# Performance work log

Hardware: AMD Instinct MI355X
Metric: run time of the kernel (lower is better)

## Reference

```python
import jax, jax.numpy as jnp
import numpy as np

NEG = -1e30  # stand-in for -inf; rows always have >=1 valid entry


def setup_inputs() -> dict:
    key = jax.random.key(0)
    ks = jax.random.split(key, 7)
    C, E, O = 256, 256, 256
    x = jax.random.normal(ks[0], (4, C, 64, 64), dtype=jnp.float32)
    # 1x1 conv weights stored as (out, in) matrices
    Wq = jax.random.normal(ks[1], (E, C), dtype=jnp.float32) * (1.0 / np.sqrt(C))
    bq = jax.random.normal(ks[2], (E,), dtype=jnp.float32) * 0.01
    Wkv = jax.random.normal(ks[3], (E + O, C), dtype=jnp.float32) * (1.0 / np.sqrt(C))
    bkv = jax.random.normal(ks[4], (E + O,), dtype=jnp.float32) * 0.01
    Wp = jax.random.normal(ks[5], (O, O), dtype=jnp.float32) * (1.0 / np.sqrt(O))
    bp = jax.random.normal(ks[6], (O,), dtype=jnp.float32) * 0.01
    return {"x": x, "Wq": Wq, "bq": bq, "Wkv": Wkv, "bkv": bkv, "Wp": Wp, "bp": bp, "n_heads": 8}


def _heads(t, n_heads):
    # (N, C, S) -> (N, n_heads, S, C//n_heads)
    n, c, s = t.shape
    return t.reshape(n, n_heads, c // n_heads, s).transpose(0, 1, 3, 2)


def reference(x, Wq, bq, Wkv, bkv, Wp, bp, n_heads):
    n, c, h, w = x.shape
    S = h * w
    E = Wq.shape[0]
    O = Wkv.shape[0] - E
    xf = x.reshape(n, c, S)  # (N, C, S)

    q = jnp.einsum('oc,ncs->nos', Wq, xf) + bq[:, None]
    kv = jnp.einsum('oc,ncs->nos', Wkv, xf) + bkv[:, None]
    k, v = kv[:, :E], kv[:, E:]

    q = _heads(q, n_heads)  # (N, H, S, dq)
    k = _heads(k, n_heads)
    v = _heads(v, n_heads)  # (N, H, S, dv)

    head_dim = E // n_heads
    # causal mask: tril with diagonal=0 (mask_center=False -> pixel attends to itself)
    mask = jnp.tril(jnp.ones((S, S), dtype=bool), k=0)

    attn = jnp.einsum('nhqd,nhkd->nhqk', q, k) / np.sqrt(head_dim)
    attn = jnp.where(mask, attn, NEG)
    attn = jax.nn.softmax(attn, axis=-1)
    attn = jnp.where(mask, attn, 0.0)

    out = jnp.einsum('nhqk,nhkd->nhqd', attn, v)  # (N, H, S, dv)
    out = out.transpose(0, 1, 3, 2).reshape(n, O, S)  # (N, O, S)
    out = jnp.einsum('oc,ncs->nos', Wp, out) + bp[:, None]
    return out.reshape(n, O, h, w)
```

## Files before the change

kernel.cpp:

```cpp
#include <hip/hip_runtime.h>

typedef __bf16 bf16x8 __attribute__((ext_vector_type(8)));
typedef float f32x4 __attribute__((ext_vector_type(4)));
typedef float f32x16 __attribute__((ext_vector_type(16)));

#define S_LEN 4096

__device__ __forceinline__ unsigned short f2bf(float f) {
    unsigned int u = __float_as_uint(f);
    u += 0x7fffu + ((u >> 16) & 1u);
    return (unsigned short)(u >> 16);
}

__device__ __forceinline__ unsigned int pk_bf16(float lo, float hi) {
    unsigned int r;
    asm("v_cvt_pk_bf16_f32 %0, %1, %2" : "=v"(r) : "v"(lo), "v"(hi));
    return r;
}

__global__ __launch_bounds__(256) void k_xt(const float* __restrict__ x, unsigned short* __restrict__ xT,
                                            const float* __restrict__ Wq, const float* __restrict__ Wkv,
                                            const float* __restrict__ Wp, unsigned short* __restrict__ wb,
                                            unsigned short* __restrict__ wpb) {
    __shared__ unsigned short tile[64 * 80];
    const int tid = threadIdx.x;
    if (blockIdx.z == 4) {
        const int bi = blockIdx.x + 64 * blockIdx.y;
        for (int i = bi * 256 + tid; i < 262144; i += 65536) {
            if (i < 65536)       wb[i]           = f2bf(Wq[i]);
            else if (i < 196608) wb[i]           = f2bf(Wkv[i - 65536]);
            else                 wpb[i - 196608] = f2bf(Wp[i - 196608]);
        }
        return;
    }
    const int b = blockIdx.z, c0 = blockIdx.y * 64, s0 = blockIdx.x * 64;
#pragma unroll
    for (int ii = 0; ii < 4; ++ii) {
        int flat = ii * 256 + tid;
        int cr = flat >> 4, s4 = flat & 15;
        const float4 v = *(const float4*)(x + ((size_t)(b * 256 + c0 + cr)) * S_LEN + s0 + s4 * 4);
        tile[(s4 * 4 + 0) * 80 + cr] = f2bf(v.x);
        tile[(s4 * 4 + 1) * 80 + cr] = f2bf(v.y);
        tile[(s4 * 4 + 2) * 80 + cr] = f2bf(v.z);
        tile[(s4 * 4 + 3) * 80 + cr] = f2bf(v.w);
    }
    __syncthreads();
#pragma unroll
    for (int ii = 0; ii < 2; ++ii) {
        int flat = ii * 256 + tid;
        int sr = flat >> 3, ch = flat & 7;
        uint4 u = *(const uint4*)&tile[sr * 80 + ch * 8];
        *(uint4*)(xT + ((size_t)(b * 4096 + s0 + sr)) * 256 + c0 + ch * 8) = u;
    }
}

__global__ __launch_bounds__(256) void k_qkv(const unsigned short* __restrict__ wb,
                                             const unsigned short* __restrict__ xT,
                                             const float* __restrict__ bq,
                                             const float* __restrict__ bkv,
                                             unsigned short* __restrict__ qws,
                                             unsigned short* __restrict__ kws,
                                             unsigned short* __restrict__ vws) {
    __shared__ unsigned short As[128 * 32];
    __shared__ unsigned short Bs[128 * 32];
    const int b = blockIdx.z;
    const int o0 = blockIdx.y * 128, s0 = blockIdx.x * 128;
    const int tid = threadIdx.x;
    const int w = tid >> 6, l = tid & 63, g = l >> 4, lc = l & 15;
    const int wr = w >> 1, wc = w & 1;
    const unsigned short* xb = xT + (size_t)b * 4096 * 256;
    const float SM_C = 0.25505654458f;

    f32x4 acc[4][4];
#pragma unroll
    for (int m = 0; m < 4; ++m)
#pragma unroll
        for (int nf = 0; nf < 4; ++nf) acc[m][nf] = (f32x4)(0.f);

    const int lrow = tid >> 1, lhalf = tid & 1;
    const int lsw0 = (lrow * 64 + lhalf * 32) ^ ((lrow & 7) << 4);
    const int lsw1 = (lrow * 64 + lhalf * 32 + 16) ^ ((lrow & 7) << 4);

    for (int kk = 0; kk < 8; ++kk) {
        const int c0 = kk * 32;
        __syncthreads();
        {
            const uint4* srcA = (const uint4*)(wb + (size_t)(o0 + lrow) * 256 + c0 + lhalf * 16);
            uint4 a0 = srcA[0], a1 = srcA[1];
            const uint4* srcB = (const uint4*)(xb + (size_t)(s0 + lrow) * 256 + c0 + lhalf * 16);
            uint4 b0 = srcB[0], b1 = srcB[1];
            *(uint4*)((char*)As + lsw0) = a0;
            *(uint4*)((char*)As + lsw1) = a1;
            *(uint4*)((char*)Bs + lsw0) = b0;
            *(uint4*)((char*)Bs + lsw1) = b1;
        }
        __syncthreads();
        bf16x8 af[4], bfv[4];
#pragma unroll
        for (int m = 0; m < 4; ++m) {
            int row = wr * 64 + m * 16 + lc;
            af[m] = *(const bf16x8*)((char*)As + ((row * 64 + g * 16) ^ ((row & 7) << 4)));
        }
#pragma unroll
        for (int nf = 0; nf < 4; ++nf) {
            int row = wc * 64 + nf * 16 + lc;
            bfv[nf] = *(const bf16x8*)((char*)Bs + ((row * 64 + g * 16) ^ ((row & 7) << 4)));
        }
#pragma unroll
        for (int m = 0; m < 4; ++m)
#pragma unroll
            for (int nf = 0; nf < 4; ++nf)
                acc[m][nf] = __builtin_amdgcn_mfma_f32_16x16x32_bf16(af[m], bfv[nf], acc[m][nf], 0, 0, 0);
    }

#pragma unroll
    for (int m = 0; m < 4; ++m)
#pragma unroll
        for (int nf = 0; nf < 4; ++nf)
#pragma unroll
            for (int i = 0; i < 4; ++i) {
                int o = o0 + wr * 64 + m * 16 + g * 4 + i;
                int s = s0 + wc * 64 + nf * 16 + lc;
                if (o < 256) {
                    int h = o >> 5, d = o & 31;
                    qws[(((size_t)(b * 8 + h)) * 4096 + s) * 32 + d] = f2bf((acc[m][nf][i] + bq[o]) * SM_C);
                } else if (o < 512) {
                    int oo = o - 256, h = oo >> 5, d = oo & 31;
                    kws[(((size_t)(b * 8 + h)) * 4096 + s) * 32 + d] = f2bf(acc[m][nf][i] + bkv[o - 256]);
                } else {
                    int oo = o - 512, h = oo >> 5, d = oo & 31;
                    vws[(size_t)(b * 8 + h) * 131072 + (((s >> 7) * 32 + d) << 7) + (s & 127)] =
                        f2bf(acc[m][nf][i] + bkv[o - 256]);
                }
            }
}

#define VC_STRIDE 544
#define BUF_STRIDE 8704

__device__ __forceinline__ void attn_sub(const unsigned short* __restrict__ kw_bh, int key0,
                                         const char* __restrict__ vbuf, int c,
                                         bf16x8 qf0, bf16x8 qf1, const f32x16& zf, bf16x8 ones,
                                         int lane31, int hh, bool domask,
                                         f32x16& o, f32x16& sums) {
    const unsigned short* kp = kw_bh + (size_t)(key0 + lane31) * 32 + hh * 8;
    bf16x8 kf0 = *(const bf16x8*)(kp);
    bf16x8 kf1 = *(const bf16x8*)(kp + 16);
    bf16x8 vf0 = *(const bf16x8*)(vbuf + (c * 4 + hh) * VC_STRIDE + lane31 * 16);
    bf16x8 vf1 = *(const bf16x8*)(vbuf + (c * 4 + 2 + hh) * VC_STRIDE + lane31 * 16);

    f32x16 s = __builtin_amdgcn_mfma_f32_32x32x16_bf16(kf0, qf0, zf, 0, 0, 0);
    s = __builtin_amdgcn_mfma_f32_32x32x16_bf16(kf1, qf1, s, 0, 0, 0);

    if (domask) {
#pragma unroll
        for (int r = 0; r < 16; ++r) {
            int krel = (r & 3) + 8 * (r >> 2) + 4 * hh;
            if (krel > lane31) s[r] = -1e30f;
        }
    }

    float p[16];
#pragma unroll
    for (int r = 0; r < 16; ++r) p[r] = __builtin_amdgcn_exp2f(s[r]);

    unsigned int c00 = pk_bf16(p[0], p[1]),   c01 = pk_bf16(p[2], p[3]);
    unsigned int c10 = pk_bf16(p[4], p[5]),   c11 = pk_bf16(p[6], p[7]);
    unsigned int c20 = pk_bf16(p[8], p[9]),   c21 = pk_bf16(p[10], p[11]);
    unsigned int c30 = pk_bf16(p[12], p[13]), c31 = pk_bf16(p[14], p[15]);
    asm("v_permlane32_swap_b32 %0, %1" : "+v"(c00), "+v"(c10));
    asm("v_permlane32_swap_b32 %0, %1" : "+v"(c01), "+v"(c11));
    asm("v_permlane32_swap_b32 %0, %1" : "+v"(c20), "+v"(c30));
    asm("v_permlane32_swap_b32 %0, %1" : "+v"(c21), "+v"(c31));
    union U { uint4 u; bf16x8 v; };
    U pa0, pa1;
    pa0.u = make_uint4(c00, c01, c10, c11);
    pa1.u = make_uint4(c20, c21, c30, c31);

    sums = __builtin_amdgcn_mfma_f32_32x32x16_bf16(ones, pa0.v, sums, 0, 0, 0);
    sums = __builtin_amdgcn_mfma_f32_32x32x16_bf16(ones, pa1.v, sums, 0, 0, 0);
    o = __builtin_amdgcn_mfma_f32_32x32x16_bf16(vf0, pa0.v, o, 0, 0, 0);
    o = __builtin_amdgcn_mfma_f32_32x32x16_bf16(vf1, pa1.v, o, 0, 0, 0);
}

__global__ __launch_bounds__(256, 4) void k_attn(const unsigned short* __restrict__ qw,
                                                 const unsigned short* __restrict__ kw,
                                                 const unsigned short* __restrict__ vw,
                                                 unsigned short* __restrict__ att) {
    __shared__ __align__(16) char smem[2 * BUF_STRIDE];

    const int tid = threadIdx.x;
    const int w = tid >> 6, l = tid & 63;
    const int lane31 = l & 31, hh = l >> 5;

    const int B = blockIdx.x;
    const int xcd = B & 7, idx = B >> 3;
    const int bh = xcd * 4 + (idx & 3);
    const int v4 = idx >> 2;
    const int j4 = v4 >> 3, d4 = v4 & 7;
    const int mt = (j4 & 1) ? (31 - 8 * (j4 >> 1) - d4) : (8 * (j4 >> 1) + d4);

    const int q = mt * 128 + w * 32 + lane31;

    const unsigned short* qw_bh = qw + (size_t)bh * 4096 * 32;
    const unsigned short* kw_bh = kw + (size_t)bh * 4096 * 32;
    const unsigned short* vw_bh = vw + (size_t)bh * 131072;

    const bf16x8 qf0 = *(const bf16x8*)(qw_bh + (size_t)q * 32 + hh * 8);
    const bf16x8 qf1 = *(const bf16x8*)(qw_bh + (size_t)q * 32 + hh * 8 + 16);

    const unsigned short* vsrc = vw_bh + tid * 16;
    const int vd0 = ((tid & 7) * 2) * VC_STRIDE + (tid >> 3) * 16;

    f32x16 o, sums, zf;
#pragma unroll
    for (int r = 0; r < 16; ++r) { o[r] = 0.f; sums[r] = 0.f; zf[r] = 0.f; }

    union OU { unsigned int u[4]; bf16x8 v; };
    OU onesU;
#pragma unroll
    for (int jj = 0; jj < 4; ++jj) onesU.u[jj] = 0x3F803F80u;
    const bf16x8 ones = onesU.v;

    {
        uint4 va = *(const uint4*)(vsrc);
        uint4 vbb = *(const uint4*)(vsrc + 8);
        *(uint4*)(smem + vd0)             = va;
        *(uint4*)(smem + vd0 + VC_STRIDE) = vbb;
    }

    int cur = 0;
    for (int r = 0; r < mt; ++r) {
        const unsigned short* vp = vsrc + (size_t)(r + 1) * 4096;
        uint4 va = *(const uint4*)(vp);
        uint4 vbb = *(const uint4*)(vp + 8);

        __syncthreads();
        const char* vbuf = smem + cur * BUF_STRIDE;
        const int k0 = r * 128;
        attn_sub(kw_bh, k0,      vbuf, 0, qf0, qf1, zf, ones, lane31, hh, false, o, sums);
        attn_sub(kw_bh, k0 + 32, vbuf, 1, qf0, qf1, zf, ones, lane31, hh, false, o, sums);
        attn_sub(kw_bh, k0 + 64, vbuf, 2, qf0, qf1, zf, ones, lane31, hh, false, o, sums);
        attn_sub(kw_bh, k0 + 96, vbuf, 3, qf0, qf1, zf, ones, lane31, hh, false, o, sums);

        char* nb = smem + (cur ^ 1) * BUF_STRIDE;
        *(uint4*)(nb + vd0)             = va;
        *(uint4*)(nb + vd0 + VC_STRIDE) = vbb;
        cur ^= 1;
    }

    __syncthreads();
    {
        const char* vbuf = smem + cur * BUF_STRIDE;
        const int k0 = mt * 128;
#pragma unroll
        for (int c = 0; c < 4; ++c)
            if (c <= w)
                attn_sub(kw_bh, k0 + 32 * c, vbuf, c, qf0, qf1, zf, ones, lane31, hh, c == w, o, sums);
    }

    const float inv = 1.0f / sums[0];
    unsigned int* dst = (unsigned int*)(att + (((size_t)(bh >> 3)) * 4096 + q) * 256 + (bh & 7) * 32);
#pragma unroll
    for (int jj = 0; jj < 8; ++jj) {
        unsigned int v = pk_bf16(o[2 * jj] * inv, o[2 * jj + 1] * inv);
        dst[(jj & 1) + 4 * (jj >> 1) + 2 * hh] = v;
    }
}

__global__ __launch_bounds__(256) void k_proj(const unsigned short* __restrict__ wpb,
                                              const unsigned short* __restrict__ att,
                                              const float* __restrict__ bp,
                                              float* __restrict__ out) {
    __shared__ unsigned short As[128 * 32];
    __shared__ unsigned short Bs[128 * 32];
    const int b = blockIdx.z;
    const int o0 = blockIdx.y * 128, s0 = blockIdx.x * 128;
    const int tid = threadIdx.x;
    const int w = tid >> 6, l = tid & 63, g = l >> 4, lc = l & 15;
    const int wr = w >> 1, wc = w & 1;
    const unsigned short* ab = att + (size_t)b * 4096 * 256;

    f32x4 acc[4][4];
#pragma unroll
    for (int m = 0; m < 4; ++m)
#pragma unroll
        for (int nf = 0; nf < 4; ++nf) acc[m][nf] = (f32x4)(0.f);

    const int lrow = tid >> 1, lhalf = tid & 1;
    const int lsw0 = (lrow * 64 + lhalf * 32) ^ ((lrow & 7) << 4);
    const int lsw1 = (lrow * 64 + lhalf * 32 + 16) ^ ((lrow & 7) << 4);

    for (int kk = 0; kk < 8; ++kk) {
        const int c0 = kk * 32;
        __syncthreads();
        {
            const uint4* srcA = (const uint4*)(wpb + (size_t)(o0 + lrow) * 256 + c0 + lhalf * 16);
            uint4 a0 = srcA[0], a1 = srcA[1];
            const uint4* srcB = (const uint4*)(ab + (size_t)(s0 + lrow) * 256 + c0 + lhalf * 16);
            uint4 b0 = srcB[0], b1 = srcB[1];
            *(uint4*)((char*)As + lsw0) = a0;
            *(uint4*)((char*)As + lsw1) = a1;
            *(uint4*)((char*)Bs + lsw0) = b0;
            *(uint4*)((char*)Bs + lsw1) = b1;
        }
        __syncthreads();
        bf16x8 af[4], bfv[4];
#pragma unroll
        for (int m = 0; m < 4; ++m) {
            int row = wr * 64 + m * 16 + lc;
            af[m] = *(const bf16x8*)((char*)As + ((row * 64 + g * 16) ^ ((row & 7) << 4)));
        }
#pragma unroll
        for (int nf = 0; nf < 4; ++nf) {
            int row = wc * 64 + nf * 16 + lc;
            bfv[nf] = *(const bf16x8*)((char*)Bs + ((row * 64 + g * 16) ^ ((row & 7) << 4)));
        }
#pragma unroll
        for (int m = 0; m < 4; ++m)
#pragma unroll
            for (int nf = 0; nf < 4; ++nf)
                acc[m][nf] = __builtin_amdgcn_mfma_f32_16x16x32_bf16(af[m], bfv[nf], acc[m][nf], 0, 0, 0);
    }

#pragma unroll
    for (int m = 0; m < 4; ++m)
#pragma unroll
        for (int nf = 0; nf < 4; ++nf)
#pragma unroll
            for (int i = 0; i < 4; ++i) {
                int o = o0 + wr * 64 + m * 16 + g * 4 + i;
                int s = s0 + wc * 64 + nf * 16 + lc;
                out[((size_t)(b * 256 + o)) * 4096 + s] = acc[m][nf][i] + bp[o];
            }
}

extern "C" void kernel_launch(void* const* d_in, const int* in_sizes, int n_in,
                              void* d_out, int out_size, void* d_ws, size_t ws_size,
                              hipStream_t stream) {
    const float* x   = (const float*)d_in[0];
    const float* Wq  = (const float*)d_in[1];
    const float* bq  = (const float*)d_in[2];
    const float* Wkv = (const float*)d_in[3];
    const float* bkv = (const float*)d_in[4];
    const float* Wp  = (const float*)d_in[5];
    const float* bp  = (const float*)d_in[6];
    float* out = (float*)d_out;
    char* ws = (char*)d_ws;

    unsigned short* wb  = (unsigned short*)(ws);
    unsigned short* wpb = (unsigned short*)(ws + 393216);
    unsigned short* xT  = (unsigned short*)(ws + 524288);
    unsigned short* qws = (unsigned short*)(ws + 8912896);
    unsigned short* kws = (unsigned short*)(ws + 17301504);
    unsigned short* vws = (unsigned short*)(ws + 25690112);
    unsigned short* att = (unsigned short*)(ws + 34078720);

    hipLaunchKernelGGL(k_xt, dim3(64, 4, 5), dim3(256), 0, stream, x, xT, Wq, Wkv, Wp, wb, wpb);
    hipLaunchKernelGGL(k_qkv, dim3(32, 6, 4), dim3(256), 0, stream, wb, xT, bq, bkv, qws, kws, vws);
    hipLaunchKernelGGL(k_attn, dim3(1024), dim3(256), 0, stream, qws, kws, vws, att);
    hipLaunchKernelGGL(k_proj, dim3(32, 2, 4), dim3(256), 0, stream, wpb, att, bp, out);
}
```

Measured before the change: 119.1 us.

## Process two V tiles per barrier and batch K fragment loads per round

The attention loop now stages two 128-key V tiles per shared-memory slot, halving the number of __syncthreads barriers per query tile, and handles an odd leftover tile in the tail. K fragments for a whole 128-key round are loaded up front into registers before the MFMA chain, so global-load latency overlaps more compute. LDS use doubles to about 34 KB per block and register pressure rises from the eight held K fragments, which may reduce occupancy under the 4-blocks-per-SM launch bound.

New measurement: 112.3 us, median of 2. -5.7%, faster.

```diff
diff --git a/kernel.cpp b/kernel.cpp
--- a/kernel.cpp
+++ b/kernel.cpp
@@ -136,16 +136,14 @@
 }
 
 #define VC_STRIDE 544
-#define BUF_STRIDE 8704
-
-__device__ __forceinline__ void attn_sub(const unsigned short* __restrict__ kw_bh, int key0,
+#define HALF_STRIDE 8704
+#define SLOT_STRIDE 17408
+
+__device__ __forceinline__ void attn_sub(bf16x8 kf0, bf16x8 kf1,
                                          const char* __restrict__ vbuf, int c,
                                          bf16x8 qf0, bf16x8 qf1, const f32x16& zf, bf16x8 ones,
                                          int lane31, int hh, bool domask,
                                          f32x16& o, f32x16& sums) {
-    const unsigned short* kp = kw_bh + (size_t)(key0 + lane31) * 32 + hh * 8;
-    bf16x8 kf0 = *(const bf16x8*)(kp);
-    bf16x8 kf1 = *(const bf16x8*)(kp + 16);
     bf16x8 vf0 = *(const bf16x8*)(vbuf + (c * 4 + hh) * VC_STRIDE + lane31 * 16);
     bf16x8 vf1 = *(const bf16x8*)(vbuf + (c * 4 + 2 + hh) * VC_STRIDE + lane31 * 16);
 
@@ -183,11 +181,28 @@
     o = __builtin_amdgcn_mfma_f32_32x32x16_bf16(vf1, pa1.v, o, 0, 0, 0);
 }
 
+__device__ __forceinline__ void attn_round_full(const unsigned short* __restrict__ kw_bh, int k0,
+                                                const char* __restrict__ vhalf,
+                                                bf16x8 qf0, bf16x8 qf1, const f32x16& zf, bf16x8 ones,
+                                                int lane31, int hh,
+                                                f32x16& o, f32x16& sums) {
+    const unsigned short* kp = kw_bh + (size_t)(k0 + lane31) * 32 + hh * 8;
+    bf16x8 kf[8];
+#pragma unroll
+    for (int c = 0; c < 4; ++c) {
+        kf[2 * c]     = *(const bf16x8*)(kp + c * 1024);
+        kf[2 * c + 1] = *(const bf16x8*)(kp + c * 1024 + 16);
+    }
+#pragma unroll
+    for (int c = 0; c < 4; ++c)
+        attn_sub(kf[2 * c], kf[2 * c + 1], vhalf, c, qf0, qf1, zf, ones, lane31, hh, false, o, sums);
+}
+
 __global__ __launch_bounds__(256, 4) void k_attn(const unsigned short* __restrict__ qw,
                                                  const unsigned short* __restrict__ kw,
                                                  const unsigned short* __restrict__ vw,
                                                  unsigned short* __restrict__ att) {
-    __shared__ __align__(16) char smem[2 * BUF_STRIDE];
+    __shared__ __align__(16) char smem[2 * SLOT_STRIDE];
 
     const int tid = threadIdx.x;
     const int w = tid >> 6, l = tid & 63;
@@ -201,6 +216,7 @@
     const int mt = (j4 & 1) ? (31 - 8 * (j4 >> 1) - d4) : (8 * (j4 >> 1) + d4);
 
     const int q = mt * 128 + w * 32 + lane31;
+    const int D = (mt + 2) >> 1;
 
     const unsigned short* qw_bh = qw + (size_t)bh * 4096 * 32;
     const unsigned short* kw_bh = kw + (size_t)bh * 4096 * 32;
@@ -223,40 +239,56 @@
     const bf16x8 ones = onesU.v;
 
     {
-        uint4 va = *(const uint4*)(vsrc);
-        uint4 vbb = *(const uint4*)(vsrc + 8);
-        *(uint4*)(smem + vd0)             = va;
-        *(uint4*)(smem + vd0 + VC_STRIDE) = vbb;
+        uint4 a0 = *(const uint4*)(vsrc);
+        uint4 a1 = *(const uint4*)(vsrc + 8);
+        uint4 b0 = *(const uint4*)(vsrc + 4096);
+        uint4 b1 = *(const uint4*)(vsrc + 4096 + 8);
+        *(uint4*)(smem + vd0)                           = a0;
+        *(uint4*)(smem + vd0 + VC_STRIDE)               = a1;
+        *(uint4*)(smem + HALF_STRIDE + vd0)             = b0;
+        *(uint4*)(smem + HALF_STRIDE + vd0 + VC_STRIDE) = b1;
     }
 
     int cur = 0;
-    for (int r = 0; r < mt; ++r) {
-        const unsigned short* vp = vsrc + (size_t)(r + 1) * 4096;
-        uint4 va = *(const uint4*)(vp);
-        uint4 vbb = *(const uint4*)(vp + 8);
-
-        __syncthreads();
-        const char* vbuf = smem + cur * BUF_STRIDE;
-        const int k0 = r * 128;
-        attn_sub(kw_bh, k0,      vbuf, 0, qf0, qf1, zf, ones, lane31, hh, false, o, sums);
-        attn_sub(kw_bh, k0 + 32, vbuf, 1, qf0, qf1, zf, ones, lane31, hh, false, o, sums);
-        attn_sub(kw_bh, k0 + 64, vbuf, 2, qf0, qf1, zf, ones, lane31, hh, false, o, sums);
-        attn_sub(kw_bh, k0 + 96, vbuf, 3, qf0, qf1, zf, ones, lane31, hh, false, o, sums);
-
-        char* nb = smem + (cur ^ 1) * BUF_STRIDE;
-        *(uint4*)(nb + vd0)             = va;
-        *(uint4*)(nb + vd0 + VC_STRIDE) = vbb;
+    for (int d = 0; d < D - 1; ++d) {
+        const unsigned short* vp = vsrc + (size_t)(d + 1) * 8192;
+        uint4 a0 = *(const uint4*)(vp);
+        uint4 a1 = *(const uint4*)(vp + 8);
+        uint4 b0 = *(const uint4*)(vp + 4096);
+        uint4 b1 = *(const uint4*)(vp + 4096 + 8);
+
+        __syncthreads();
+        const char* vbase = smem + cur * SLOT_STRIDE;
+        attn_round_full(kw_bh, 256 * d,       vbase,               qf0, qf1, zf, ones, lane31, hh, o, sums);
+        attn_round_full(kw_bh, 256 * d + 128, vbase + HALF_STRIDE, qf0, qf1, zf, ones, lane31, hh, o, sums);
+
+        char* nb = smem + (cur ^ 1) * SLOT_STRIDE;
+        *(uint4*)(nb + vd0)                           = a0;
+        *(uint4*)(nb + vd0 + VC_STRIDE)               = a1;
+        *(uint4*)(nb + HALF_STRIDE + vd0)             = b0;
+        *(uint4*)(nb + HALF_STRIDE + vd0 + VC_STRIDE) = b1;
         cur ^= 1;
     }
 
     __syncthreads();
     {
-        const char* vbuf = smem + cur * BUF_STRIDE;
-        const int k0 = mt * 128;
+        const char* vbase = smem + cur * SLOT_STRIDE;
+        const char* dv = vbase;
+        if (mt & 1) {
+            attn_round_full(kw_bh, 128 * (mt - 1), vbase, qf0, qf1, zf, ones, lane31, hh, o, sums);
+            dv = vbase + HALF_STRIDE;
+        }
+        const unsigned short* kp = kw_bh + (size_t)(128 * mt + lane31) * 32 + hh * 8;
+        bf16x8 kf[8];
+#pragma unroll
+        for (int c = 0; c < 4; ++c) {
+            kf[2 * c]     = *(const bf16x8*)(kp + c * 1024);
+            kf[2 * c + 1] = *(const bf16x8*)(kp + c * 1024 + 16);
+        }
 #pragma unroll
         for (int c = 0; c < 4; ++c)
             if (c <= w)
-                attn_sub(kw_bh, k0 + 32 * c, vbuf, c, qf0, qf1, zf, ones, lane31, hh, c == w, o, sums);
+                attn_sub(kf[2 * c], kf[2 * c + 1], dv, c, qf0, qf1, zf, ones, lane31, hh, c == w, o, sums);
     }
 
     const float inv = 1.0f / sums[0];
```

## Split long causal query tiles into two key-range halves with a combine kernel

Applied to the files above, without the earlier changes.

Query tiles in the upper half of the causal triangle (mt>=16) are now split across two blocks, each covering about half the key range. Partial unnormalized outputs and row sums go to workspace (reusing the xT area), and a new k_combine kernel adds them and normalizes. The goal is to balance per-block work and cut the tail of the triangular schedule, at the cost of an extra launch, extra memory traffic and an extra bf16 rounding of partial outputs. K fragments for a 128-key tile are also loaded up front, before the MFMAs, to improve latency hiding.

After: 122.7 us. 3.0% more time.

```diff
diff --git a/kernel.cpp b/kernel.cpp
--- a/kernel.cpp
+++ b/kernel.cpp
@@ -16,6 +16,10 @@
     unsigned int r;
     asm("v_cvt_pk_bf16_f32 %0, %1, %2" : "=v"(r) : "v"(lo), "v"(hi));
     return r;
+}
+
+__device__ __forceinline__ float bf2f(unsigned int hw) {
+    return __uint_as_float(hw << 16);
 }
 
 __global__ __launch_bounds__(256) void k_xt(const float* __restrict__ x, unsigned short* __restrict__ xT,
@@ -138,14 +142,11 @@
 #define VC_STRIDE 544
 #define BUF_STRIDE 8704
 
-__device__ __forceinline__ void attn_sub(const unsigned short* __restrict__ kw_bh, int key0,
+__device__ __forceinline__ void attn_sub(bf16x8 kf0, bf16x8 kf1,
                                          const char* __restrict__ vbuf, int c,
                                          bf16x8 qf0, bf16x8 qf1, const f32x16& zf, bf16x8 ones,
                                          int lane31, int hh, bool domask,
                                          f32x16& o, f32x16& sums) {
-    const unsigned short* kp = kw_bh + (size_t)(key0 + lane31) * 32 + hh * 8;
-    bf16x8 kf0 = *(const bf16x8*)(kp);
-    bf16x8 kf1 = *(const bf16x8*)(kp + 16);
     bf16x8 vf0 = *(const bf16x8*)(vbuf + (c * 4 + hh) * VC_STRIDE + lane31 * 16);
     bf16x8 vf1 = *(const bf16x8*)(vbuf + (c * 4 + 2 + hh) * VC_STRIDE + lane31 * 16);
 
@@ -186,7 +187,9 @@
 __global__ __launch_bounds__(256, 4) void k_attn(const unsigned short* __restrict__ qw,
                                                  const unsigned short* __restrict__ kw,
                                                  const unsigned short* __restrict__ vw,
-                                                 unsigned short* __restrict__ att) {
+                                                 unsigned short* __restrict__ att,
+                                                 unsigned int* __restrict__ pox0,
+                                                 float* __restrict__ psums) {
     __shared__ __align__(16) char smem[2 * BUF_STRIDE];
 
     const int tid = threadIdx.x;
@@ -196,9 +199,21 @@
     const int B = blockIdx.x;
     const int xcd = B & 7, idx = B >> 3;
     const int bh = xcd * 4 + (idx & 3);
-    const int v4 = idx >> 2;
-    const int j4 = v4 >> 3, d4 = v4 & 7;
-    const int mt = (j4 & 1) ? (31 - 8 * (j4 >> 1) - d4) : (8 * (j4 >> 1) + d4);
+    const int j = idx >> 2;
+
+    int mt, r0, rlast, part0 = -1, half = 0;
+    bool diag;
+    if (j < 16) {
+        mt = j; r0 = 0; rlast = mt; diag = true;
+    } else {
+        const int jj = j - 16;
+        mt = 16 + (jj >> 1);
+        half = jj & 1;
+        const int h = (mt + 1) >> 1;
+        if (half == 0) { r0 = 0; rlast = h - 1; diag = false; }
+        else           { r0 = h; rlast = mt;    diag = true;  }
+        part0 = bh * 16 + (mt - 16);
+    }
 
     const int q = mt * 128 + w * 32 + lane31;
 
@@ -219,29 +234,35 @@
     union OU { unsigned int u[4]; bf16x8 v; };
     OU onesU;
 #pragma unroll
-    for (int jj = 0; jj < 4; ++jj) onesU.u[jj] = 0x3F803F80u;
+    for (int jj2 = 0; jj2 < 4; ++jj2) onesU.u[jj2] = 0x3F803F80u;
     const bf16x8 ones = onesU.v;
 
     {
-        uint4 va = *(const uint4*)(vsrc);
-        uint4 vbb = *(const uint4*)(vsrc + 8);
+        const unsigned short* vp = vsrc + (size_t)r0 * 4096;
+        uint4 va = *(const uint4*)(vp);
+        uint4 vbb = *(const uint4*)(vp + 8);
         *(uint4*)(smem + vd0)             = va;
         *(uint4*)(smem + vd0 + VC_STRIDE) = vbb;
     }
 
     int cur = 0;
-    for (int r = 0; r < mt; ++r) {
+    for (int r = r0; r < rlast; ++r) {
         const unsigned short* vp = vsrc + (size_t)(r + 1) * 4096;
         uint4 va = *(const uint4*)(vp);
         uint4 vbb = *(const uint4*)(vp + 8);
 
         __syncthreads();
         const char* vbuf = smem + cur * BUF_STRIDE;
-        const int k0 = r * 128;
-        attn_sub(kw_bh, k0,      vbuf, 0, qf0, qf1, zf, ones, lane31, hh, false, o, sums);
-        attn_sub(kw_bh, k0 + 32, vbuf, 1, qf0, qf1, zf, ones, lane31, hh, false, o, sums);
-        attn_sub(kw_bh, k0 + 64, vbuf, 2, qf0, qf1, zf, ones, lane31, hh, false, o, sums);
-        attn_sub(kw_bh, k0 + 96, vbuf, 3, qf0, qf1, zf, ones, lane31, hh, false, o, sums);
+        const unsigned short* kp = kw_bh + (size_t)(r * 128 + lane31) * 32 + hh * 8;
+        bf16x8 kf[8];
+#pragma unroll
+        for (int c = 0; c < 4; ++c) {
+            kf[2 * c]     = *(const bf16x8*)(kp + c * 1024);
+            kf[2 * c + 1] = *(const bf16x8*)(kp + c * 1024 + 16);
+        }
+#pragma unroll
+        for (int c = 0; c < 4; ++c)
+            attn_sub(kf[2 * c], kf[2 * c + 1], vbuf, c, qf0, qf1, zf, ones, lane31, hh, false, o, sums);
 
         char* nb = smem + (cur ^ 1) * BUF_STRIDE;
         *(uint4*)(nb + vd0)             = va;
@@ -252,19 +273,71 @@
     __syncthreads();
     {
         const char* vbuf = smem + cur * BUF_STRIDE;
-        const int k0 = mt * 128;
-#pragma unroll
-        for (int c = 0; c < 4; ++c)
-            if (c <= w)
-                attn_sub(kw_bh, k0 + 32 * c, vbuf, c, qf0, qf1, zf, ones, lane31, hh, c == w, o, sums);
-    }
-
-    const float inv = 1.0f / sums[0];
+        const unsigned short* kp = kw_bh + (size_t)(rlast * 128 + lane31) * 32 + hh * 8;
+        bf16x8 kf[8];
+#pragma unroll
+        for (int c = 0; c < 4; ++c) {
+            kf[2 * c]     = *(const bf16x8*)(kp + c * 1024);
+            kf[2 * c + 1] = *(const bf16x8*)(kp + c * 1024 + 16);
+        }
+        if (diag) {
+#pragma unroll
+            for (int c = 0; c < 4; ++c)
+                if (c <= w)
+                    attn_sub(kf[2 * c], kf[2 * c + 1], vbuf, c, qf0, qf1, zf, ones, lane31, hh, c == w, o, sums);
+        } else {
+#pragma unroll
+            for (int c = 0; c < 4; ++c)
+                attn_sub(kf[2 * c], kf[2 * c + 1], vbuf, c, qf0, qf1, zf, ones, lane31, hh, false, o, sums);
+        }
+    }
+
+    if (part0 < 0) {
+        const float inv = 1.0f / sums[0];
+        unsigned int* dst = (unsigned int*)(att + (((size_t)(bh >> 3)) * 4096 + q) * 256 + (bh & 7) * 32);
+#pragma unroll
+        for (int jj2 = 0; jj2 < 8; ++jj2) {
+            unsigned int v = pk_bf16(o[2 * jj2] * inv, o[2 * jj2 + 1] * inv);
+            dst[(jj2 & 1) + 4 * (jj2 >> 1) + 2 * hh] = v;
+        }
+    } else if (half == 0) {
+        unsigned int* po = pox0 + ((size_t)part0 * 256 + tid) * 8;
+#pragma unroll
+        for (int jj2 = 0; jj2 < 8; ++jj2)
+            po[jj2] = pk_bf16(o[2 * jj2], o[2 * jj2 + 1]);
+        psums[(size_t)(part0 * 2) * 256 + tid] = sums[0];
+    } else {
+        unsigned int* dst = (unsigned int*)(att + (((size_t)(bh >> 3)) * 4096 + q) * 256 + (bh & 7) * 32);
+#pragma unroll
+        for (int jj2 = 0; jj2 < 8; ++jj2)
+            dst[(jj2 & 1) + 4 * (jj2 >> 1) + 2 * hh] = pk_bf16(o[2 * jj2], o[2 * jj2 + 1]);
+        psums[(size_t)(part0 * 2 + 1) * 256 + tid] = sums[0];
+    }
+}
+
+__global__ __launch_bounds__(256) void k_combine(const unsigned int* __restrict__ pox0,
+                                                 const float* __restrict__ psums,
+                                                 unsigned short* __restrict__ att) {
+    const int C = blockIdx.x;
+    const int bh = C >> 4, mt = 16 + (C & 15);
+    const int part0 = bh * 16 + (mt - 16);
+    const int tid = threadIdx.x;
+    const int w = tid >> 6, l = tid & 63;
+    const int lane31 = l & 31, hh = l >> 5;
+
+    const unsigned int* p0 = pox0 + ((size_t)part0 * 256 + tid) * 8;
+    const float sum = psums[(size_t)(part0 * 2) * 256 + tid] + psums[(size_t)(part0 * 2 + 1) * 256 + tid];
+    const float inv = 1.0f / sum;
+
+    const int q = mt * 128 + w * 32 + lane31;
     unsigned int* dst = (unsigned int*)(att + (((size_t)(bh >> 3)) * 4096 + q) * 256 + (bh & 7) * 32);
 #pragma unroll
     for (int jj = 0; jj < 8; ++jj) {
-        unsigned int v = pk_bf16(o[2 * jj] * inv, o[2 * jj + 1] * inv);
-        dst[(jj & 1) + 4 * (jj >> 1) + 2 * hh] = v;
+        const int di = (jj & 1) + 4 * (jj >> 1) + 2 * hh;
+        unsigned int u0 = p0[jj], u1 = dst[di];
+        float lo = bf2f(u0 & 0xffffu) + bf2f(u1 & 0xffffu);
+        float hi = bf2f(u0 >> 16) + bf2f(u1 >> 16);
+        dst[di] = pk_bf16(lo * inv, hi * inv);
     }
 }
 
@@ -355,9 +428,12 @@
     unsigned short* kws = (unsigned short*)(ws + 17301504);
     unsigned short* vws = (unsigned short*)(ws + 25690112);
     unsigned short* att = (unsigned short*)(ws + 34078720);
+    unsigned int*   pox0  = (unsigned int*)(ws + 524288);
+    float*          psums = (float*)(ws + 524288 + 4194304);
 
     hipLaunchKernelGGL(k_xt, dim3(64, 4, 5), dim3(256), 0, stream, x, xT, Wq, Wkv, Wp, wb, wpb);
     hipLaunchKernelGGL(k_qkv, dim3(32, 6, 4), dim3(256), 0, stream, wb, xT, bq, bkv, qws, kws, vws);
-    hipLaunchKernelGGL(k_attn, dim3(1024), dim3(256), 0, stream, qws, kws, vws, att);
+    hipLaunchKernelGGL(k_attn, dim3(1536), dim3(256), 0, stream, qws, kws, vws, att, pox0, psums);
+    hipLaunchKernelGGL(k_combine, dim3(512), dim3(256), 0, stream, pox0, psums, att);
     hipLaunchKernelGGL(k_proj, dim3(32, 2, 4), dim3(256), 0, stream, wpb, att, bp, out);
 }
```
